# Performance work log

Hardware: AMD Instinct MI355X
Metric: run time of the kernel (lower is better)

Reference implementation:

```python
import jax, jax.numpy as jnp
import numpy as np
from math import factorial

N_NODES = 100000
N_EDGES = 1600000
HIDDEN = 8
N_GRAPHS = 64
RC = 1.5            # PolynomialCutoff radius
CUT_P = 6           # polynomial cutoff exponent (DimeNet-style)
GB_SIGMA = 0.1      # GaussianBasisExpansion width
GB_NUM = 10
GB_LO, GB_HI = 0.7, 1.7
LN2 = 0.6931471805599453

def _cgc(j1, m1, j2, m2, j3, m3):
    if m1 + m2 != m3:
        return 0.0
    f = factorial
    pre = ((2*j3+1) * f(j3+j1-j2) * f(j3-j1+j2) * f(j1+j2-j3) / f(j1+j2+j3+1)) ** 0.5
    pre *= (f(j3+m3)*f(j3-m3)*f(j1-m1)*f(j1+m1)*f(j2-m2)*f(j2+m2)) ** 0.5
    s = 0.0
    for k in range(max(0, j2-j3-m1, j1-j3+m2), min(j1+j2-j3, j1-m1, j2+m2) + 1):
        s += (-1)**k / (f(k)*f(j1+j2-j3-k)*f(j1-m1-k)*f(j2+m2-k)*f(j3-j2+m1+k)*f(j3-j1-m2+k))
    return pre * s

def _u(l):
    # complex -> real spherical-harmonic change of basis; rows indexed by real m = -l..l
    U = np.zeros((2*l+1, 2*l+1), dtype=complex)
    U[l, l] = 1.0
    for m in range(1, l+1):
        U[l+m, l+m] = (-1)**m / np.sqrt(2.0)
        U[l+m, l-m] = 1.0 / np.sqrt(2.0)
        U[l-m, l-m] = 1j / np.sqrt(2.0)
        U[l-m, l+m] = -1j * (-1)**m / np.sqrt(2.0)
    return U

def _real_cg(l1, l2, l3):
    cgc = np.zeros((2*l1+1, 2*l2+1, 2*l3+1), dtype=complex)
    for m1 in range(-l1, l1+1):
        for m2 in range(-l2, l2+1):
            m3 = m1 + m2
            if -l3 <= m3 <= l3:
                cgc[l1+m1, l2+m2, l3+m3] = _cgc(l1, m1, l2, m2, l3, m3)
    W = np.einsum('ai,bj,ck,ijk->cab', _u(l1), _u(l2), np.conj(_u(l3)), cgc)
    re, im = np.real(W), np.imag(W)
    w = re if np.abs(re).sum() >= np.abs(im).sum() else im
    return jnp.asarray(w, dtype=jnp.float32)  # (2l3+1, 2l1+1, 2l2+1)

_TRIPLES = [(0,0,0),(0,1,1),(1,0,1),(1,1,0),(1,1,1),(1,2,1)]
CG = {t: _real_cg(*t) for t in _TRIPLES}
PATHS1 = [(0,0,0),(0,1,1)]                                    # L_in=0, L_edge=2, L_out=1
PATHS2 = [(0,0,0),(0,1,1),(1,0,1),(1,1,0),(1,1,1),(1,2,1)]    # L_in=1, L_edge=2, L_out=1
PATHS3 = [(0,0,0),(1,1,0)]                                    # L_in=1, L_edge=2, L_out=0
DEG_L1 = jnp.array([0, 1, 1, 1])  # degree of each order slot for L = 0..1
DEG_L0 = jnp.array([0])

def _ssp(x):
    return jax.nn.softplus(x) - LN2

def _so3_linear(x, sh, w, paths, n_out_orders, channel_wise):
    # x: (E, in_orders, Cin); sh: (E, edge_orders); w: (E,P,C) or (E,P,Cin,Cout)
    E = x.shape[0]
    c_out = w.shape[-1]
    out = jnp.zeros((E, n_out_orders, c_out), x.dtype)
    for p, (l1, l2, l3) in enumerate(paths):
        cg = CG[(l1, l2, l3)]                      # (2l3+1, 2l1+1, 2l2+1)
        xs = x[:, l1*l1:(l1+1)**2, :]
        ss = sh[:, l2*l2:(l2+1)**2]
        m = jnp.einsum('oab,eac,eb->eoc', cg, xs, ss)
        if channel_wise:
            m = m * w[:, p][:, None, :]
        else:
            m = jnp.einsum('eoc,ecd->eod', m, w[:, p])
        out = out.at[:, l3*l3:(l3+1)**2, :].add(m)
    return out

def _norm_act(h, act, degs):
    # NormAct: per-degree, per-channel norm gating x * act(||x||) / ||x||
    parts = []
    for l in degs:
        seg = h[:, l*l:(l+1)**2, :]
        n = jnp.sqrt(jnp.sum(seg*seg, axis=1, keepdims=True) + 1e-12)
        parts.append(seg * (act(n) / n))
    return jnp.concatenate(parts, axis=1)

def _tfn_block(x, src, dst, sh, edge_emb, edge_w, wp_w, wp_b, si_w, paths, n_out_orders, channel_wise, deg_idx):
    E = sh.shape[0]
    c_in = x.shape[-1]
    lw = edge_emb @ wp_w + wp_b                  # weight_producer (per-edge CG path weights)
    P = len(paths)
    if channel_wise:
        lw = lw.reshape(E, P, c_in)
    else:
        lw = lw.reshape(E, P, c_in, -1)
    msg = _so3_linear(x[src], sh, lw, paths, n_out_orders, channel_wise)  # gather + CG TP
    msg = msg * edge_w[:, None, None]
    agg = jax.ops.segment_sum(msg, dst, num_segments=N_NODES)             # scatter-sum
    return jnp.einsum('nmc,mcd->nmd', agg, si_w[deg_idx])                 # DegreeWiseLinear self-interaction

def _forward(x, edge_index, edge_sh, edge_len, batch, wp1_w, wp1_b, wp2_w, wp2_b, wp3_w, wp3_b, si1_w, si2_w, si3_w, out_w, out_b):
    src, dst = edge_index[0], edge_index[1]
    centers = jnp.linspace(GB_LO, GB_HI, GB_NUM)
    edge_emb = jnp.exp(-(edge_len[:, None] - centers[None, :])**2 / (2.0 * GB_SIGMA**2))
    u = edge_len / RC
    p = CUT_P
    cut = 1.0 - (p+1)*(p+2)/2.0*u**p + p*(p+2)*u**(p+1) - p*(p+1)/2.0*u**(p+2)
    edge_w = jnp.where(u < 1.0, cut, 0.0)
    h = x[:, None, :]                                   # (N, 1 order, 1 channel)
    h = _tfn_block(h, src, dst, edge_sh, edge_emb, edge_w, wp1_w, wp1_b, si1_w, PATHS1, 4, False, DEG_L1)
    h = _norm_act(h, _ssp, (0, 1))
    h = _tfn_block(h, src, dst, edge_sh, edge_emb, edge_w, wp2_w, wp2_b, si2_w, PATHS2, 4, True, DEG_L1)
    h = _norm_act(h, _ssp, (0, 1))
    h = _tfn_block(h, src, dst, edge_sh, edge_emb, edge_w, wp3_w, wp3_b, si3_w, PATHS3, 1, True, DEG_L0)
    h = jax.nn.silu(h)
    g = jax.ops.segment_sum(h[:, 0, :], batch, num_segments=N_GRAPHS)   # SumAggregation pool
    return jax.nn.softmax(g @ out_w + out_b, axis=-1)

def setup_inputs():
    key = jax.random.key(0)
    ks = jax.random.split(key, 16)
    H = HIDDEN
    s = lambda k, shp: jax.random.normal(k, shp, jnp.float32) * 0.1
    return {
        'x': jax.random.normal(ks[0], (N_NODES, 1), jnp.float32),
        'edge_index': jax.random.randint(ks[1], (2, N_EDGES), 0, N_NODES),
        'edge_sh': jax.random.normal(ks[2], (N_EDGES, 9), jnp.float32),
        'edge_len': jax.random.uniform(ks[3], (N_EDGES,), jnp.float32) * 1.5,
        'batch': jnp.sort(jax.random.randint(ks[4], (N_NODES,), 0, N_GRAPHS)),
        'wp1_w': s(ks[5], (10, 2*H)), 'wp1_b': jnp.zeros((2*H,), jnp.float32),
        'wp2_w': s(ks[6], (10, 6*H)), 'wp2_b': jnp.zeros((6*H,), jnp.float32),
        'wp3_w': s(ks[7], (10, 2*H)), 'wp3_b': jnp.zeros((2*H,), jnp.float32),
        'si1_w': s(ks[8], (2, H, H)), 'si2_w': s(ks[9], (2, H, H)), 'si3_w': s(ks[10], (1, H, H)),
        'out_w': s(ks[11], (H, 8)), 'out_b': jnp.zeros((8,), jnp.float32),
    }

def reference(x, edge_index, edge_sh, edge_len, batch, wp1_w, wp1_b, wp2_w, wp2_b, wp3_w, wp3_b, si1_w, si2_w, si3_w, out_w, out_b):
    return _forward(x, edge_index, edge_sh, edge_len, batch, wp1_w, wp1_b, wp2_w, wp2_b, wp3_w, wp3_b, si1_w, si2_w, si3_w, out_w, out_b)
```

## Files before the change

kernel.cpp:

```cpp
#include <hip/hip_runtime.h>
#include <hip/hip_fp16.h>
#include <math.h>
#include <complex>

#define NN 100000
#define NE 1600000
#define NG 64
#define TBINS 256
#define NBLK_E   6250
#define NBLK_N8  3125
#define NBLK_SCAN 391

struct CGTables {
  float c000;
  float c011[3][3];
  float c101[3][3];
  float c110[3][3];
  float c111[3][3][3];
  float c121[3][3][5];
};
struct CGConsts {
  float c000;
  float l011, l101, l110, l111;
  float s121[5][5];
};

static double hfact(int n){ double r=1.0; for(int i=2;i<=n;++i) r*=(double)i; return r; }

static double host_cgc(int j1,int m1,int j2,int m2,int j3,int m3){
  if (m1+m2 != m3) return 0.0;
  double pre = sqrt((2.0*j3+1.0)*hfact(j3+j1-j2)*hfact(j3-j1+j2)*hfact(j1+j2-j3)/hfact(j1+j2+j3+1));
  pre *= sqrt(hfact(j3+m3)*hfact(j3-m3)*hfact(j1-m1)*hfact(j1+m1)*hfact(j2-m2)*hfact(j2+m2));
  int k0 = 0; if (j2-j3-m1 > k0) k0 = j2-j3-m1; if (j1-j3+m2 > k0) k0 = j1-j3+m2;
  int k1 = j1+j2-j3; if (j1-m1 < k1) k1 = j1-m1; if (j2+m2 < k1) k1 = j2+m2;
  double s = 0.0;
  for (int k=k0;k<=k1;++k){
    double t = 1.0/(hfact(k)*hfact(j1+j2-j3-k)*hfact(j1-m1-k)*hfact(j2+m2-k)*hfact(j3-j2+m1+k)*hfact(j3-j1-m2+k));
    s += (k&1) ? -t : t;
  }
  return pre*s;
}

typedef std::complex<double> cd;

static void host_u(int l, cd U[5][5]){
  for (int a=0;a<5;++a) for (int b=0;b<5;++b) U[a][b] = 0.0;
  U[l][l] = 1.0;
  const double is2 = 1.0/sqrt(2.0);
  for (int m=1;m<=l;++m){
    double sgn = (m&1) ? -1.0 : 1.0;
    U[l+m][l+m] = sgn*is2;
    U[l+m][l-m] = is2;
    U[l-m][l-m] = cd(0.0, is2);
    U[l-m][l+m] = cd(0.0, -sgn*is2);
  }
}

static void host_real_cg(int l1,int l2,int l3, float* out){
  cd U1[5][5], U2[5][5], U3[5][5];
  host_u(l1,U1); host_u(l2,U2); host_u(l3,U3);
  int n1=2*l1+1, n2=2*l2+1, n3=2*l3+1;
  double cgt[5][5][5];
  for (int i=0;i<5;++i) for (int j=0;j<5;++j) for (int k=0;k<5;++k) cgt[i][j][k]=0.0;
  for (int m1=-l1;m1<=l1;++m1) for (int m2=-l2;m2<=l2;++m2){
    int m3 = m1+m2;
    if (m3 >= -l3 && m3 <= l3) cgt[l1+m1][l2+m2][l3+m3] = host_cgc(l1,m1,l2,m2,l3,m3);
  }
  cd W[5][5][5];
  double sre=0.0, sim=0.0;
  for (int c=0;c<n3;++c) for (int a=0;a<n1;++a) for (int b=0;b<n2;++b){
    cd acc = 0.0;
    for (int i=0;i<n1;++i) for (int j=0;j<n2;++j) for (int k=0;k<n3;++k)
      acc += U1[a][i]*U2[b][j]*std::conj(U3[c][k])*cgt[i][j][k];
    W[c][a][b] = acc;
    sre += fabs(acc.real()); sim += fabs(acc.imag());
  }
  bool use_re = (sre >= sim);
  for (int c=0;c<n3;++c) for (int a=0;a<n1;++a) for (int b=0;b<n2;++b)
    out[(c*n1+a)*n2+b] = (float)(use_re ? W[c][a][b].real() : W[c][a][b].imag());
}

static void build_cg_tables(CGTables& t){
  float w000[1];  host_real_cg(0,0,0,w000); t.c000 = w000[0];
  float w011[9];  host_real_cg(0,1,1,w011);
  for (int o=0;o<3;++o) for (int b=0;b<3;++b) t.c011[o][b] = w011[o*3+b];
  float w101[9];  host_real_cg(1,0,1,w101);
  for (int o=0;o<3;++o) for (int a=0;a<3;++a) t.c101[o][a] = w101[o*3+a];
  float w110[9];  host_real_cg(1,1,0,w110);
  for (int a=0;a<3;++a) for (int b=0;b<3;++b) t.c110[a][b] = w110[a*3+b];
  float w111[27]; host_real_cg(1,1,1,w111);
  for (int o=0;o<3;++o) for (int a=0;a<3;++a) for (int b=0;b<3;++b) t.c111[o][a][b] = w111[(o*3+a)*3+b];
  float w121[45]; host_real_cg(1,2,1,w121);
  for (int o=0;o<3;++o) for (int a=0;a<3;++a) for (int b=0;b<5;++b) t.c121[o][a][b] = w121[(o*3+a)*5+b];
}

static void build_cg_consts(const CGTables& t, CGConsts& K){
  K.c000 = t.c000;
  K.l011 = t.c011[0][0];
  K.l101 = t.c101[0][0];
  K.l110 = t.c110[0][0];
  K.l111 = t.c111[0][1][2];
  const int pi[5] = {0,0,0,1,1};
  const int pj[5] = {0,1,2,1,2};
  for (int p=0;p<5;++p)
    for (int b=0;b<5;++b)
      K.s121[p][b] = 0.5f*(t.c121[pi[p]][pj[p]][b] + t.c121[pj[p]][pi[p]][b]);
}

__device__ __forceinline__ float sspf(float v){
  float sp = (v > 30.0f) ? v : log1pf(expf(v));
  return sp - 0.69314718055994531f;
}

__device__ __forceinline__ float cutoff_w(float len){
  float u = len * (1.0f/1.5f);
  float u2 = u*u, u6 = u2*u2*u2, u7 = u6*u, u8 = u7*u;
  float cut = 1.0f - 28.0f*u6 + 48.0f*u7 - 21.0f*u8;
  return (u < 1.0f) ? cut : 0.0f;
}

__device__ __forceinline__ float pack2h(float a, float b){
  __half2 h = __floats2half2_rn(a, b);
  return *reinterpret_cast<float*>(&h);
}
__device__ __forceinline__ float2 unpack2h(float f){
  __half2 h = *reinterpret_cast<__half2*>(&f);
  return __half22float2(h);
}

__global__ __launch_bounds__(256) void lwtab_kernel(
    const float* __restrict__ wpw, const float* __restrict__ wpb,
    int NP, float* __restrict__ tab)
{
  int idx = blockIdx.x*256 + threadIdx.x;
  int tot = TBINS*NP*8;
  if (idx >= tot) return;
  int stride = NP*8;
  int bin = idx / stride;
  int r = idx - bin*stride;
  float len = (1.5f/(TBINS-1)) * bin;
  float v = wpb[r];
  #pragma unroll
  for (int i=0;i<10;++i){
    float dd = len - (0.7f + (float)i*(1.0f/9.0f));
    v = fmaf(wpw[i*stride + r], __expf(-50.0f*dd*dd), v);
  }
  tab[idx] = v;
}

__global__ __launch_bounds__(256) void hist_kernel(const int* __restrict__ dst, int* __restrict__ hist){
  int e = blockIdx.x*256 + threadIdx.x;
  if (e >= NE) return;
  atomicAdd(&hist[dst[e]], 1);
}

__global__ __launch_bounds__(256) void scan1_kernel(const int* __restrict__ hist, int* __restrict__ bsum){
  __shared__ int s[256];
  int i = blockIdx.x*256 + threadIdx.x;
  int t = threadIdx.x;
  s[t] = (i < NN) ? hist[i] : 0;
  __syncthreads();
  for (int off=128; off>0; off>>=1){ if (t < off) s[t] += s[t+off]; __syncthreads(); }
  if (t == 0) bsum[blockIdx.x] = s[0];
}

__global__ __launch_bounds__(512) void scan2_kernel(const int* __restrict__ bsum, int* __restrict__ boff){
  __shared__ int s[512];
  int t = threadIdx.x;
  int v = (t < NBLK_SCAN) ? bsum[t] : 0;
  s[t] = v; __syncthreads();
  for (int off=1; off<512; off<<=1){
    int u = (t >= off) ? s[t-off] : 0;
    __syncthreads();
    s[t] += u;
    __syncthreads();
  }
  if (t < NBLK_SCAN) boff[t] = s[t] - v;
}

__global__ __launch_bounds__(256) void scan3_kernel(const int* __restrict__ hist, const int* __restrict__ boff,
                                                   int* __restrict__ rowptr, int* __restrict__ cursor){
  __shared__ int s[256];
  int i = blockIdx.x*256 + threadIdx.x;
  int t = threadIdx.x;
  int v = (i < NN) ? hist[i] : 0;
  s[t] = v; __syncthreads();
  for (int off=1; off<256; off<<=1){
    int u = (t >= off) ? s[t-off] : 0;
    __syncthreads();
    s[t] += u;
    __syncthreads();
  }
  int excl = s[t] - v + boff[blockIdx.x];
  if (i < NN){ rowptr[i] = excl; cursor[i] = excl; }
  if (i == 0) rowptr[NN] = NE;
}

__global__ __launch_bounds__(256) void deg_hist_kernel(const int* __restrict__ rowptr, int* __restrict__ dcnt){
  __shared__ int lb[256];
  lb[threadIdx.x] = 0; __syncthreads();
  int n = blockIdx.x*256 + threadIdx.x;
  if (n < NN){
    int d = rowptr[n+1]-rowptr[n]; if (d > 255) d = 255;
    atomicAdd(&lb[d], 1);
  }
  __syncthreads();
  if (lb[threadIdx.x]) atomicAdd(&dcnt[threadIdx.x], lb[threadIdx.x]);
}

__global__ void deg_scan_kernel(const int* __restrict__ dcnt, int* __restrict__ dcur){
  __shared__ int s[256];
  int t = threadIdx.x;
  int v = dcnt[t];
  s[t] = v; __syncthreads();
  for (int off=1; off<256; off<<=1){
    int u = (t >= off) ? s[t-off] : 0;
    __syncthreads();
    s[t] += u;
    __syncthreads();
  }
  dcur[t] = s[t] - v;
}

__global__ __launch_bounds__(256) void deg_scatter_kernel(const int* __restrict__ rowptr,
                                                          int* __restrict__ dcur, int* __restrict__ perm){
  __shared__ int lcnt[256];
  __shared__ int lbase[256];
  int t = threadIdx.x;
  lcnt[t] = 0;
  __syncthreads();
  int n = blockIdx.x*256 + t;
  int d = 0, lrank = 0;
  bool valid = (n < NN);
  if (valid){
    d = rowptr[n+1]-rowptr[n]; if (d > 255) d = 255;
    lrank = atomicAdd(&lcnt[d], 1);
  }
  __syncthreads();
  int cnt = lcnt[t];
  if (cnt > 0) lbase[t] = atomicAdd(&dcur[t], cnt);
  __syncthreads();
  if (valid) perm[lbase[d] + lrank] = n;
}

__global__ __launch_bounds__(256) void scatter_rec_kernel(
    const int* __restrict__ src, const int* __restrict__ dst,
    const float* __restrict__ sh, const float* __restrict__ elen,
    const float* __restrict__ x,
    int* __restrict__ cursor, float4* __restrict__ rec, CGConsts K)
{
  int e = blockIdx.x*256 + threadIdx.x;
  if (e >= NE) return;
  float len = elen[e];
  float w = cutoff_w(len);
  const float* shr = sh + (size_t)e*9;
  float sh0 = shr[0]*w, shx = shr[1]*w, shy = shr[2]*w, shz = shr[3]*w;
  float b0 = shr[4], b1 = shr[5], b2 = shr[6], b3 = shr[7], b4 = shr[8];
  float S[5];
  #pragma unroll
  for (int p=0;p<5;++p)
    S[p] = (K.s121[p][0]*b0 + K.s121[p][1]*b1 + K.s121[p][2]*b2 + K.s121[p][3]*b3 + K.s121[p][4]*b4)*w;
  int sn = src[e];
  float x0 = x[sn];
  int d = dst[e];
  int slot = atomicAdd(&cursor[d], 1);
  float4* rp = rec + (size_t)slot*2;
  rp[0] = make_float4(__int_as_float(sn), len, pack2h(sh0, shx), pack2h(shy, shz));
  rp[1] = make_float4(pack2h(S[0], S[1]), pack2h(S[2], S[3]), S[4], x0);
}

__global__ __launch_bounds__(256) void gather1_kernel(
    const int* __restrict__ rowptr, const int* __restrict__ perm,
    const float4* __restrict__ rec, const float* __restrict__ tab,
    const float* __restrict__ si, float* __restrict__ out, CGConsts K)
{
  __shared__ float lwt[TBINS*16];
  for (int i=threadIdx.x; i<TBINS*16; i+=256) lwt[i] = tab[i];
  __syncthreads();
  int gid = blockIdx.x*256 + threadIdx.x;
  int c = gid & 7;
  int n = perm[gid >> 3];
  int r0 = rowptr[n], r1 = rowptr[n+1];
  float a0=0.f, a1=0.f, a2=0.f, a3=0.f;
  #pragma unroll 2
  for (int s=r0; s<r1; ++s){
    const float4* rp = rec + (size_t)s*2;
    float4 q0 = rp[0];
    float4 q1 = rp[1];
    float len = q0.y;
    float2 s01 = unpack2h(q0.z);
    float2 s23 = unpack2h(q0.w);
    float sh0 = s01.x, shx = s01.y, shy = s23.x, shz = s23.y;
    float x0 = q1.w;
    float fb = len * ((TBINS-1)/1.5f);
    int bin = (int)fb; if (bin > TBINS-2) bin = TBINS-2;
    float fr = fb - (float)bin;
    int tb = bin*16 + c;
    float lw0 = fmaf(fr, lwt[tb+16]-lwt[tb], lwt[tb]);
    float lw1 = fmaf(fr, lwt[tb+24]-lwt[tb+8], lwt[tb+8]);
    a0 = fmaf(K.c000*sh0, x0*lw0, a0);
    float t = K.l011*x0*lw1;
    a1 = fmaf(t, shx, a1); a2 = fmaf(t, shy, a2); a3 = fmaf(t, shz, a3);
  }
  float z0=0.f, z1=0.f, z2=0.f, z3=0.f;
  #pragma unroll
  for (int k=0;k<8;++k){
    float y0 = __shfl(a0,k,8), y1 = __shfl(a1,k,8), y2 = __shfl(a2,k,8), y3 = __shfl(a3,k,8);
    float w0 = si[k*8+c], w1 = si[64+k*8+c];
    z0 = fmaf(y0,w0,z0); z1 = fmaf(y1,w1,z1); z2 = fmaf(y2,w1,z2); z3 = fmaf(y3,w1,z3);
  }
  float n0 = sqrtf(z0*z0 + 1e-12f);
  float r0v = z0*(sspf(n0)/n0);
  float nv = sqrtf(z1*z1 + z2*z2 + z3*z3 + 1e-12f);
  float sc = sspf(nv)/nv;
  float4 o = make_float4(r0v, z1*sc, z2*sc, z3*sc);
  *reinterpret_cast<float4*>(out + ((size_t)n*8 + c)*4) = o;
}

__global__ __launch_bounds__(256) void gather2_kernel(
    const float* __restrict__ hin,
    const int* __restrict__ rowptr, const int* __restrict__ perm,
    const float4* __restrict__ rec, const float* __restrict__ tab,
    const float* __restrict__ si, float* __restrict__ out, CGConsts K)
{
  __shared__ float lwt[TBINS*48];
  for (int i=threadIdx.x; i<TBINS*48; i+=256) lwt[i] = tab[i];
  __syncthreads();
  int gid = blockIdx.x*256 + threadIdx.x;
  int c = gid & 7;
  int n = perm[gid >> 3];
  int r0 = rowptr[n], r1 = rowptr[n+1];
  float a0=0.f, a1=0.f, a2=0.f, a3=0.f;
  #pragma unroll 2
  for (int s=r0; s<r1; ++s){
    const float4* rp = rec + (size_t)s*2;
    float4 q0 = rp[0];
    float4 q1 = rp[1];
    int sn = __float_as_int(q0.x);
    float len = q0.y;
    float2 s01 = unpack2h(q0.z);
    float2 s23 = unpack2h(q0.w);
    float sh0 = s01.x, shx = s01.y, shy = s23.x, shz = s23.y;
    float2 Sa = unpack2h(q1.x);
    float2 Sb = unpack2h(q1.y);
    float S00 = Sa.x, S01 = Sa.y, S02 = Sb.x, S11 = Sb.y, S12 = q1.z;
    float S22 = -S00 - S11;
    float4 hv = *reinterpret_cast<const float4*>(hin + ((size_t)sn*8 + c)*4);
    float x0 = hv.x, xa0 = hv.y, xa1 = hv.z, xa2 = hv.w;
    float fb = len * ((TBINS-1)/1.5f);
    int bin = (int)fb; if (bin > TBINS-2) bin = TBINS-2;
    float fr = fb - (float)bin;
    int tb = bin*48 + c;
    float lw[6];
    #pragma unroll
    for (int p=0;p<6;++p){
      float t0v = lwt[tb + p*8];
      float t1v = lwt[tb + 48 + p*8];
      lw[p] = fmaf(fr, t1v - t0v, t0v);
    }
    float shdotx = shx*xa0 + shy*xa1 + shz*xa2;
    a0 += K.c000*sh0*x0*lw[0] + K.l110*shdotx*lw[3];
    float t011 = K.l011*x0*lw[1];
    float t101 = K.l101*sh0*lw[2];
    float l4 = K.l111*lw[4];
    float sx0 = S00*xa0 + S01*xa1 + S02*xa2;
    float sx1 = S01*xa0 + S11*xa1 + S12*xa2;
    float sx2 = S02*xa0 + S12*xa1 + S22*xa2;
    a1 += t011*shx + t101*xa0 + l4*(xa1*shz - xa2*shy) + sx0*lw[5];
    a2 += t011*shy + t101*xa1 + l4*(xa2*shx - xa0*shz) + sx1*lw[5];
    a3 += t011*shz + t101*xa2 + l4*(xa0*shy - xa1*shx) + sx2*lw[5];
  }
  float z0=0.f, z1=0.f, z2=0.f, z3=0.f;
  #pragma unroll
  for (int k=0;k<8;++k){
    float y0 = __shfl(a0,k,8), y1 = __shfl(a1,k,8), y2 = __shfl(a2,k,8), y3 = __shfl(a3,k,8);
    float w0 = si[k*8+c], w1 = si[64+k*8+c];
    z0 = fmaf(y0,w0,z0); z1 = fmaf(y1,w1,z1); z2 = fmaf(y2,w1,z2); z3 = fmaf(y3,w1,z3);
  }
  float n0 = sqrtf(z0*z0 + 1e-12f);
  float r0v = z0*(sspf(n0)/n0);
  float nv = sqrtf(z1*z1 + z2*z2 + z3*z3 + 1e-12f);
  float sc = sspf(nv)/nv;
  float4 o = make_float4(r0v, z1*sc, z2*sc, z3*sc);
  *reinterpret_cast<float4*>(out + ((size_t)n*8 + c)*4) = o;
}

__global__ __launch_bounds__(256) void gather3_kernel(
    const float* __restrict__ hin, const int* __restrict__ rowptr, const int* __restrict__ perm,
    const float4* __restrict__ rec, const float* __restrict__ tab,
    const float* __restrict__ si, const int* __restrict__ batch,
    float* __restrict__ G, CGConsts K)
{
  __shared__ float lwt[TBINS*16];
  __shared__ float lg[512];
  for (int i=threadIdx.x; i<TBINS*16; i+=256) lwt[i] = tab[i];
  lg[threadIdx.x] = 0.f; lg[256+threadIdx.x] = 0.f;
  __syncthreads();
  int gid = blockIdx.x*256 + threadIdx.x;
  int c = gid & 7;
  int n = perm[gid >> 3];
  int r0 = rowptr[n], r1 = rowptr[n+1];
  float acc = 0.f;
  #pragma unroll 2
  for (int s=r0; s<r1; ++s){
    float4 q0 = rec[(size_t)s*2];
    int sn = __float_as_int(q0.x);
    float len = q0.y;
    float2 s01 = unpack2h(q0.z);
    float2 s23 = unpack2h(q0.w);
    float sh0 = s01.x, shx = s01.y, shy = s23.x, shz = s23.y;
    float4 hv = *reinterpret_cast<const float4*>(hin + ((size_t)sn*8 + c)*4);
    float fb = len * ((TBINS-1)/1.5f);
    int bin = (int)fb; if (bin > TBINS-2) bin = TBINS-2;
    float fr = fb - (float)bin;
    int tb = bin*16 + c;
    float lw0 = fmaf(fr, lwt[tb+16]-lwt[tb], lwt[tb]);
    float lw1 = fmaf(fr, lwt[tb+24]-lwt[tb+8], lwt[tb+8]);
    float shdotx = shx*hv.y + shy*hv.z + shz*hv.w;
    acc += K.c000*sh0*hv.x*lw0 + K.l110*shdotx*lw1;
  }
  float z = 0.f;
  #pragma unroll
  for (int k=0;k<8;++k){
    float y = __shfl(acc,k,8);
    z = fmaf(y, si[k*8+c], z);
  }
  float v = z / (1.0f + expf(-z));
  atomicAdd(&lg[batch[n]*8 + c], v);
  __syncthreads();
  int t = threadIdx.x;
  float v0 = lg[t];     if (v0 != 0.f) unsafeAtomicAdd(&G[t], v0);
  float v1 = lg[256+t]; if (v1 != 0.f) unsafeAtomicAdd(&G[256+t], v1);
}

__global__ void final_kernel(
    const float* __restrict__ g, const float* __restrict__ ow,
    const float* __restrict__ ob, float* __restrict__ out)
{
  int i = threadIdx.x;
  if (i >= NG) return;
  float gv[8];
  #pragma unroll
  for (int c=0;c<8;++c) gv[c] = g[i*8+c];
  float lg[8];
  #pragma unroll
  for (int j=0;j<8;++j){
    float acc = ob[j];
    #pragma unroll
    for (int c=0;c<8;++c) acc += gv[c]*ow[c*8+j];
    lg[j] = acc;
  }
  float mx = lg[0];
  #pragma unroll
  for (int j=1;j<8;++j) mx = fmaxf(mx, lg[j]);
  float ssum = 0.0f;
  #pragma unroll
  for (int j=0;j<8;++j){ lg[j] = expf(lg[j]-mx); ssum += lg[j]; }
  float inv = 1.0f/ssum;
  #pragma unroll
  for (int j=0;j<8;++j) out[i*8+j] = lg[j]*inv;
}

__global__ __launch_bounds__(256) void edge1_kernel(
    const float* __restrict__ x, const int* __restrict__ src, const int* __restrict__ dst,
    const float* __restrict__ sh, const float* __restrict__ elen,
    const float* __restrict__ wpw, const float* __restrict__ wpb,
    float* __restrict__ agg, CGTables cg)
{
  __shared__ float sw[176];
  for (int i=threadIdx.x;i<176;i+=256) sw[i] = (i<160) ? wpw[i] : wpb[i-160];
  __syncthreads();
  int e = blockIdx.x*256 + threadIdx.x;
  if (e >= NE) return;
  float len = elen[e];
  float lw[16];
  #pragma unroll
  for (int j=0;j<16;++j) lw[j] = sw[160+j];
  #pragma unroll
  for (int i=0;i<10;++i){
    float dd = len - (0.7f + (float)i*(1.0f/9.0f));
    float em = __expf(-50.0f*dd*dd);
    #pragma unroll
    for (int j=0;j<16;++j) lw[j] += em*sw[i*16+j];
  }
  float w = cutoff_w(len);
  int s = src[e], d = dst[e];
  float x0 = x[s];
  const float* shr = sh + (size_t)e*9;
  float sh0 = shr[0], sh1 = shr[1], sh2 = shr[2], sh3 = shr[3];
  float* ag = agg + (size_t)d*32;
  float b0 = cg.c000*x0*sh0*w;
  #pragma unroll
  for (int j=0;j<8;++j) unsafeAtomicAdd(ag+j, b0*lw[j]);
  #pragma unroll
  for (int o=0;o<3;++o){
    float s011 = cg.c011[o][0]*sh1 + cg.c011[o][1]*sh2 + cg.c011[o][2]*sh3;
    float bo = s011*x0*w;
    #pragma unroll
    for (int j=0;j<8;++j) unsafeAtomicAdd(ag+(1+o)*8+j, bo*lw[8+j]);
  }
}

__global__ __launch_bounds__(256) void edge2_kernel(
    const float* __restrict__ h, const int* __restrict__ src, const int* __restrict__ dst,
    const float* __restrict__ sh, const float* __restrict__ elen,
    const float* __restrict__ wpw, const float* __restrict__ wpb,
    float* __restrict__ agg, CGTables cg)
{
  __shared__ float sw[528];
  for (int i=threadIdx.x;i<528;i+=256) sw[i] = (i<480) ? wpw[i] : wpb[i-480];
  __syncthreads();
  int e = blockIdx.x*256 + threadIdx.x;
  if (e >= NE) return;
  float len = elen[e];
  float lw[48];
  #pragma unroll
  for (int j=0;j<48;++j) lw[j] = sw[480+j];
  #pragma unroll
  for (int i=0;i<10;++i){
    float dd = len - (0.7f + (float)i*(1.0f/9.0f));
    float em = __expf(-50.0f*dd*dd);
    #pragma unroll
    for (int j=0;j<48;++j) lw[j] += em*sw[i*48+j];
  }
  float w = cutoff_w(len);
  int s = src[e], d = dst[e];
  float shv[9];
  const float* shr = sh + (size_t)e*9;
  #pragma unroll
  for (int i=0;i<9;++i) shv[i] = shr[i];
  float sh0 = shv[0];
  float s011[3], k110[3], k111[3][3], k121[3][3];
  #pragma unroll
  for (int o=0;o<3;++o) s011[o] = cg.c011[o][0]*shv[1] + cg.c011[o][1]*shv[2] + cg.c011[o][2]*shv[3];
  #pragma unroll
  for (int a=0;a<3;++a) k110[a] = cg.c110[a][0]*shv[1] + cg.c110[a][1]*shv[2] + cg.c110[a][2]*shv[3];
  #pragma unroll
  for (int o=0;o<3;++o)
    #pragma unroll
    for (int a=0;a<3;++a)
      k111[o][a] = cg.c111[o][a][0]*shv[1] + cg.c111[o][a][1]*shv[2] + cg.c111[o][a][2]*shv[3];
  #pragma unroll
  for (int o=0;o<3;++o)
    #pragma unroll
    for (int a=0;a<3;++a){
      float acc = 0.0f;
      #pragma unroll
      for (int b=0;b<5;++b) acc += cg.c121[o][a][b]*shv[4+b];
      k121[o][a] = acc;
    }
  const float4* hr = reinterpret_cast<const float4*>(h + (size_t)s*32);
  float xs[32];
  #pragma unroll
  for (int i=0;i<8;++i){
    float4 q = hr[i];
    xs[i*4] = q.x; xs[i*4+1] = q.y; xs[i*4+2] = q.z; xs[i*4+3] = q.w;
  }
  float* ag = agg + (size_t)d*32;
  #pragma unroll
  for (int c=0;c<8;++c){
    float x0 = xs[c], x1 = xs[8+c], x2 = xs[16+c], x3 = xs[24+c];
    float r0 = cg.c000*sh0*x0*lw[c]
             + (k110[0]*x1 + k110[1]*x2 + k110[2]*x3)*lw[24+c];
    unsafeAtomicAdd(ag+c, r0*w);
    #pragma unroll
    for (int o=0;o<3;++o){
      float r = s011[o]*x0*lw[8+c]
              + (cg.c101[o][0]*x1 + cg.c101[o][1]*x2 + cg.c101[o][2]*x3)*sh0*lw[16+c]
              + (k111[o][0]*x1 + k111[o][1]*x2 + k111[o][2]*x3)*lw[32+c]
              + (k121[o][0]*x1 + k121[o][1]*x2 + k121[o][2]*x3)*lw[40+c];
      unsafeAtomicAdd(ag+(1+o)*8+c, r*w);
    }
  }
}

__global__ __launch_bounds__(256) void edge3_kernel(
    const float* __restrict__ h, const int* __restrict__ src, const int* __restrict__ dst,
    const float* __restrict__ sh, const float* __restrict__ elen,
    const float* __restrict__ wpw, const float* __restrict__ wpb,
    float* __restrict__ agg, CGTables cg)
{
  __shared__ float sw[176];
  for (int i=threadIdx.x;i<176;i+=256) sw[i] = (i<160) ? wpw[i] : wpb[i-160];
  __syncthreads();
  int e = blockIdx.x*256 + threadIdx.x;
  if (e >= NE) return;
  float len = elen[e];
  float lw[16];
  #pragma unroll
  for (int j=0;j<16;++j) lw[j] = sw[160+j];
  #pragma unroll
  for (int i=0;i<10;++i){
    float dd = len - (0.7f + (float)i*(1.0f/9.0f));
    float em = __expf(-50.0f*dd*dd);
    #pragma unroll
    for (int j=0;j<16;++j) lw[j] += em*sw[i*16+j];
  }
  float w = cutoff_w(len);
  int s = src[e], d = dst[e];
  const float* shr = sh + (size_t)e*9;
  float sh0 = shr[0], sh1 = shr[1], sh2 = shr[2], sh3 = shr[3];
  float k110[3];
  #pragma unroll
  for (int a=0;a<3;++a) k110[a] = cg.c110[a][0]*sh1 + cg.c110[a][1]*sh2 + cg.c110[a][2]*sh3;
  const float4* hr = reinterpret_cast<const float4*>(h + (size_t)s*32);
  float xs[32];
  #pragma unroll
  for (int i=0;i<8;++i){
    float4 q = hr[i];
    xs[i*4] = q.x; xs[i*4+1] = q.y; xs[i*4+2] = q.z; xs[i*4+3] = q.w;
  }
  float* ag = agg + (size_t)d*8;
  #pragma unroll
  for (int c=0;c<8;++c){
    float r = cg.c000*sh0*xs[c]*lw[c]
            + (k110[0]*xs[8+c] + k110[1]*xs[16+c] + k110[2]*xs[24+c])*lw[8+c];
    unsafeAtomicAdd(ag+c, r*w);
  }
}

__global__ __launch_bounds__(256) void node_fb_kernel(
    const float* __restrict__ agg, const float* __restrict__ si,
    float* __restrict__ out)
{
  __shared__ float s_si[128];
  if (threadIdx.x < 128) s_si[threadIdx.x] = si[threadIdx.x];
  __syncthreads();
  int idx = blockIdx.x*256 + threadIdx.x;
  if (idx >= NN*8) return;
  int n = idx >> 3, d = idx & 7;
  const float* ar = agg + (size_t)n*32;
  float y[4];
  #pragma unroll
  for (int m=0;m<4;++m){
    const float* sm = s_si + (m ? 64 : 0);
    float acc = 0.0f;
    #pragma unroll
    for (int c=0;c<8;++c) acc += ar[m*8+c]*sm[c*8+d];
    y[m] = acc;
  }
  float n0 = sqrtf(y[0]*y[0] + 1e-12f);
  float r0 = y[0]*(sspf(n0)/n0);
  float n1 = sqrtf(y[1]*y[1] + y[2]*y[2] + y[3]*y[3] + 1e-12f);
  float sc = sspf(n1)/n1;
  float* orow = out + (size_t)n*32;
  orow[d]      = r0;
  orow[8+d]    = y[1]*sc;
  orow[16+d]   = y[2]*sc;
  orow[24+d]   = y[3]*sc;
}

__global__ __launch_bounds__(256) void node3_fb_kernel(
    const float* __restrict__ agg, const float* __restrict__ si,
    const int* __restrict__ batch, float* __restrict__ g)
{
  __shared__ float s_si[64];
  if (threadIdx.x < 64) s_si[threadIdx.x] = si[threadIdx.x];
  __syncthreads();
  int n = blockIdx.x*256 + threadIdx.x;
  if (n >= NN) return;
  const float* ar = agg + (size_t)n*8;
  float av[8];
  #pragma unroll
  for (int c=0;c<8;++c) av[c] = ar[c];
  int b = batch[n];
  float* gr = g + (size_t)b*8;
  #pragma unroll
  for (int d=0;d<8;++d){
    float acc = 0.0f;
    #pragma unroll
    for (int c=0;c<8;++c) acc += av[c]*s_si[c*8+d];
    float v = acc / (1.0f + expf(-acc));
    unsafeAtomicAdd(gr+d, v);
  }
}

extern "C" void kernel_launch(void* const* d_in, const int* in_sizes, int n_in,
                              void* d_out, int out_size, void* d_ws, size_t ws_size,
                              hipStream_t stream)
{
  const float* x     = (const float*)d_in[0];
  const int*   eidx  = (const int*)  d_in[1];
  const float* esh   = (const float*)d_in[2];
  const float* elen  = (const float*)d_in[3];
  const int*   batch = (const int*)  d_in[4];
  const float* wp1w  = (const float*)d_in[5];
  const float* wp1b  = (const float*)d_in[6];
  const float* wp2w  = (const float*)d_in[7];
  const float* wp2b  = (const float*)d_in[8];
  const float* wp3w  = (const float*)d_in[9];
  const float* wp3b  = (const float*)d_in[10];
  const float* si1   = (const float*)d_in[11];
  const float* si2   = (const float*)d_in[12];
  const float* si3   = (const float*)d_in[13];
  const float* outw  = (const float*)d_in[14];
  const float* outb  = (const float*)d_in[15];
  const int* src = eidx;
  const int* dst = eidx + NE;

  CGTables cg;
  build_cg_tables(cg);
  CGConsts K;
  build_cg_consts(cg, K);

  char* p = (char*)d_ws;
  auto carve = [&](size_t bytes) -> void* {
    void* r = (void*)p;
    p += ((bytes + 255)/256)*256;
    return r;
  };
  int*    rowptr = (int*)   carve((NN+1)*4);
  int*    cursor = (int*)   carve(NN*4);
  int*    hist   = (int*)   carve(NN*4);
  int*    perm   = (int*)   carve(NN*4);
  int*    bsum   = (int*)   carve(512*4);
  int*    boff   = (int*)   carve(512*4);
  int*    dcnt   = (int*)   carve(256*4);
  int*    dcur   = (int*)   carve(256*4);
  float*  tab1   = (float*) carve(TBINS*16*4);
  float*  tab2   = (float*) carve(TBINS*48*4);
  float*  tab3   = (float*) carve(TBINS*16*4);
  float4* rec    = (float4*)carve((size_t)NE*32);
  float*  B1     = (float*) carve((size_t)NN*32*4);
  float*  B2     = (float*) carve((size_t)NN*32*4);
  float*  G      = (float*) carve(512*4);
  size_t need = (size_t)(p - (char*)d_ws);

  if (ws_size >= need){
    hipMemsetAsync(hist, 0, NN*sizeof(int), stream);
    hipMemsetAsync(dcnt, 0, 256*sizeof(int), stream);
    hipMemsetAsync(G, 0, 512*sizeof(float), stream);
    lwtab_kernel<<<(TBINS*16+255)/256, 256, 0, stream>>>(wp1w, wp1b, 2, tab1);
    lwtab_kernel<<<(TBINS*48+255)/256, 256, 0, stream>>>(wp2w, wp2b, 6, tab2);
    lwtab_kernel<<<(TBINS*16+255)/256, 256, 0, stream>>>(wp3w, wp3b, 2, tab3);
    hist_kernel<<<NBLK_E, 256, 0, stream>>>(dst, hist);
    scan1_kernel<<<NBLK_SCAN, 256, 0, stream>>>(hist, bsum);
    scan2_kernel<<<1, 512, 0, stream>>>(bsum, boff);
    scan3_kernel<<<NBLK_SCAN, 256, 0, stream>>>(hist, boff, rowptr, cursor);
    deg_hist_kernel<<<NBLK_SCAN, 256, 0, stream>>>(rowptr, dcnt);
    deg_scan_kernel<<<1, 256, 0, stream>>>(dcnt, dcur);
    deg_scatter_kernel<<<NBLK_SCAN, 256, 0, stream>>>(rowptr, dcur, perm);
    scatter_rec_kernel<<<NBLK_E, 256, 0, stream>>>(src, dst, esh, elen, x, cursor, rec, K);
    gather1_kernel<<<NBLK_N8, 256, 0, stream>>>(rowptr, perm, rec, tab1, si1, B1, K);
    gather2_kernel<<<NBLK_N8, 256, 0, stream>>>(B1, rowptr, perm, rec, tab2, si2, B2, K);
    gather3_kernel<<<NBLK_N8, 256, 0, stream>>>(B2, rowptr, perm, rec, tab3, si3, batch, G, K);
    final_kernel<<<1, 64, 0, stream>>>(G, outw, outb, (float*)d_out);
  } else {
    float* A  = (float*)d_ws;
    float* Bf = A + (size_t)NN*32;
    float* Cf = Bf + (size_t)NN*32;
    float* Gf = Cf + (size_t)NN*8;
    hipMemsetAsync(A, 0, (size_t)NN*32*sizeof(float), stream);
    edge1_kernel<<<NBLK_E, 256, 0, stream>>>(x, src, dst, esh, elen, wp1w, wp1b, A, cg);
    node_fb_kernel<<<(NN*8+255)/256, 256, 0, stream>>>(A, si1, Bf);
    hipMemsetAsync(A, 0, (size_t)NN*32*sizeof(float), stream);
    edge2_kernel<<<NBLK_E, 256, 0, stream>>>(Bf, src, dst, esh, elen, wp2w, wp2b, A, cg);
    node_fb_kernel<<<(NN*8+255)/256, 256, 0, stream>>>(A, si2, Bf);
    hipMemsetAsync(Cf, 0, (size_t)NN*8*sizeof(float), stream);
    edge3_kernel<<<NBLK_E, 256, 0, stream>>>(Bf, src, dst, esh, elen, wp3w, wp3b, Cf, cg);
    hipMemsetAsync(Gf, 0, (size_t)NG*8*sizeof(float), stream);
    node3_fb_kernel<<<(NN+255)/256, 256, 0, stream>>>(Cf, si3, batch, Gf);
    final_kernel<<<1, 64, 0, stream>>>(Gf, outw, outb, (float*)d_out);
  }
}
```

Measured before the change: 314.9 us.

## Replace per-node atomic CSR build with two-level bucket sort of edge records

Builds the destination-sorted edge records in two passes: a coarse bucket histogram/scan over 128-node buckets, a block-local scatter into bucket ranges, then a per-bucket in-shared-memory counting sort that writes the final sorted records and rowptr. The aim is to remove the global per-node atomic histogram, the three-kernel scan, and the fully random per-edge scatter writes, replacing them with more coherent writes at the cost of an extra full copy of the edge records. The local destination index is packed into the upper bits of the source index, so gathers now mask it out. It also halves the layer-2 radial lookup table resolution, which shrinks shared memory but changes interpolation accuracy slightly.

```diff
diff --git a/kernel.cpp b/kernel.cpp
--- a/kernel.cpp
+++ b/kernel.cpp
@@ -6,7 +6,12 @@
 #define NN 100000
 #define NE 1600000
 #define NG 64
+#define NBUCK 782
+#define SCB 256
+#define SEB 6250
 #define TBINS 256
+#define TB2   128
+#define MAXB  2560
 #define NBLK_E   6250
 #define NBLK_N8  3125
 #define NBLK_SCAN 391
@@ -130,15 +135,15 @@
 
 __global__ __launch_bounds__(256) void lwtab_kernel(
     const float* __restrict__ wpw, const float* __restrict__ wpb,
-    int NP, float* __restrict__ tab)
+    int NP, int bins, float* __restrict__ tab)
 {
   int idx = blockIdx.x*256 + threadIdx.x;
-  int tot = TBINS*NP*8;
+  int tot = bins*NP*8;
   if (idx >= tot) return;
   int stride = NP*8;
   int bin = idx / stride;
   int r = idx - bin*stride;
-  float len = (1.5f/(TBINS-1)) * bin;
+  float len = (1.5f/(bins-1)) * bin;
   float v = wpb[r];
   #pragma unroll
   for (int i=0;i<10;++i){
@@ -148,52 +153,129 @@
   tab[idx] = v;
 }
 
-__global__ __launch_bounds__(256) void hist_kernel(const int* __restrict__ dst, int* __restrict__ hist){
-  int e = blockIdx.x*256 + threadIdx.x;
-  if (e >= NE) return;
-  atomicAdd(&hist[dst[e]], 1);
-}
-
-__global__ __launch_bounds__(256) void scan1_kernel(const int* __restrict__ hist, int* __restrict__ bsum){
-  __shared__ int s[256];
-  int i = blockIdx.x*256 + threadIdx.x;
+__global__ __launch_bounds__(256) void bhist_kernel(const int* __restrict__ dst, int* __restrict__ bcnt){
+  __shared__ int cnt[NBUCK];
+  for (int j=threadIdx.x; j<NBUCK; j+=256) cnt[j] = 0;
+  __syncthreads();
+  int base = blockIdx.x * SEB;
+  for (int i=threadIdx.x; i<SEB; i+=256)
+    atomicAdd(&cnt[dst[base+i] >> 7], 1);
+  __syncthreads();
+  for (int j=threadIdx.x; j<NBUCK; j+=256)
+    if (cnt[j]) atomicAdd(&bcnt[j], cnt[j]);
+}
+
+__global__ __launch_bounds__(1024) void bscan_kernel(const int* __restrict__ bcnt,
+                                                     int* __restrict__ bbase, int* __restrict__ bclaim){
+  __shared__ int s[1024];
   int t = threadIdx.x;
-  s[t] = (i < NN) ? hist[i] : 0;
-  __syncthreads();
-  for (int off=128; off>0; off>>=1){ if (t < off) s[t] += s[t+off]; __syncthreads(); }
-  if (t == 0) bsum[blockIdx.x] = s[0];
-}
-
-__global__ __launch_bounds__(512) void scan2_kernel(const int* __restrict__ bsum, int* __restrict__ boff){
-  __shared__ int s[512];
-  int t = threadIdx.x;
-  int v = (t < NBLK_SCAN) ? bsum[t] : 0;
+  int v = (t < NBUCK) ? bcnt[t] : 0;
   s[t] = v; __syncthreads();
-  for (int off=1; off<512; off<<=1){
+  for (int off=1; off<1024; off<<=1){
     int u = (t >= off) ? s[t-off] : 0;
     __syncthreads();
     s[t] += u;
     __syncthreads();
   }
-  if (t < NBLK_SCAN) boff[t] = s[t] - v;
-}
-
-__global__ __launch_bounds__(256) void scan3_kernel(const int* __restrict__ hist, const int* __restrict__ boff,
-                                                   int* __restrict__ rowptr, int* __restrict__ cursor){
-  __shared__ int s[256];
-  int i = blockIdx.x*256 + threadIdx.x;
+  if (t < NBUCK){
+    int excl = s[t] - v;
+    bbase[t] = excl;
+    bclaim[t] = excl;
+    if (t == NBUCK-1) bbase[NBUCK] = excl + v;
+  }
+}
+
+__global__ __launch_bounds__(256) void scatter_rec_kernel(
+    const int* __restrict__ src, const int* __restrict__ dst,
+    const float* __restrict__ sh, const float* __restrict__ elen,
+    const float* __restrict__ x,
+    int* __restrict__ bclaim, float4* __restrict__ rec, CGConsts K)
+{
+  __shared__ int cnt[NBUCK];
+  __shared__ int bs[NBUCK];
+  for (int j=threadIdx.x; j<NBUCK; j+=256) cnt[j] = 0;
+  __syncthreads();
+  int base = blockIdx.x * SEB;
+  for (int i=threadIdx.x; i<SEB; i+=256)
+    atomicAdd(&cnt[dst[base+i] >> 7], 1);
+  __syncthreads();
+  for (int j=threadIdx.x; j<NBUCK; j+=256){
+    int c = cnt[j];
+    if (c) bs[j] = atomicAdd(&bclaim[j], c);
+    cnt[j] = 0;
+  }
+  __syncthreads();
+  for (int i=threadIdx.x; i<SEB; i+=256){
+    int e = base + i;
+    int d = dst[e];
+    int b = d >> 7;
+    int off = atomicAdd(&cnt[b], 1);
+    int slot = bs[b] + off;
+    float len = elen[e];
+    float w = cutoff_w(len);
+    const float* shr = sh + (size_t)e*9;
+    float sh0 = shr[0]*w, shx = shr[1]*w, shy = shr[2]*w, shz = shr[3]*w;
+    float b0 = shr[4], b1 = shr[5], b2 = shr[6], b3 = shr[7], b4 = shr[8];
+    float S[5];
+    #pragma unroll
+    for (int p=0;p<5;++p)
+      S[p] = (K.s121[p][0]*b0 + K.s121[p][1]*b1 + K.s121[p][2]*b2 + K.s121[p][3]*b3 + K.s121[p][4]*b4)*w;
+    int sn = src[e];
+    float x0 = x[sn];
+    int packed = sn | ((d & 127) << 20);
+    float4* rp = rec + (size_t)slot*2;
+    rp[0] = make_float4(__int_as_float(packed), len, pack2h(sh0, shx), pack2h(shy, shz));
+    rp[1] = make_float4(pack2h(S[0], S[1]), pack2h(S[2], S[3]), S[4], x0);
+  }
+}
+
+__global__ __launch_bounds__(256) void sortcopy_kernel(
+    const float4* __restrict__ recin, const int* __restrict__ bbase,
+    float4* __restrict__ recout, int* __restrict__ rowptr)
+{
+  __shared__ int hist[128], offs[128], cur[128];
+  __shared__ short outmap[MAXB];
+  int b = blockIdx.x;
+  int e0 = bbase[b], e1 = bbase[b+1];
+  int cnt = e1 - e0;
   int t = threadIdx.x;
-  int v = (i < NN) ? hist[i] : 0;
-  s[t] = v; __syncthreads();
-  for (int off=1; off<256; off<<=1){
-    int u = (t >= off) ? s[t-off] : 0;
+  if (t < 128) hist[t] = 0;
+  __syncthreads();
+  for (int i=t; i<cnt; i+=256){
+    int packed = __float_as_int(recin[(size_t)(e0+i)*2].x);
+    atomicAdd(&hist[packed >> 20], 1);
+  }
+  __syncthreads();
+  if (t < 128) offs[t] = hist[t];
+  __syncthreads();
+  for (int off=1; off<128; off<<=1){
+    int v = (t < 128 && t >= off) ? offs[t-off] : 0;
     __syncthreads();
-    s[t] += u;
+    if (t < 128) offs[t] += v;
     __syncthreads();
   }
-  int excl = s[t] - v + boff[blockIdx.x];
-  if (i < NN){ rowptr[i] = excl; cursor[i] = excl; }
-  if (i == 0) rowptr[NN] = NE;
+  int n0 = b << 7;
+  int nn = NN - n0; if (nn > 128) nn = 128;
+  if (t < 128){
+    int excl = offs[t] - hist[t];
+    cur[t] = excl;
+    if (t < nn) rowptr[n0+t] = e0 + excl;
+  }
+  if (b == NBUCK-1 && t == 0) rowptr[NN] = NE;
+  __syncthreads();
+  for (int i=t; i<cnt; i+=256){
+    int packed = __float_as_int(recin[(size_t)(e0+i)*2].x);
+    int r = atomicAdd(&cur[packed >> 20], 1);
+    outmap[r] = (short)i;
+  }
+  __syncthreads();
+  for (int o=t; o<cnt; o+=256){
+    int j = outmap[o];
+    const float4* rin = recin + (size_t)(e0+j)*2;
+    float4* rout = recout + (size_t)(e0+o)*2;
+    float4 a = rin[0], bq = rin[1];
+    rout[0] = a; rout[1] = bq;
+  }
 }
 
 __global__ __launch_bounds__(256) void deg_hist_kernel(const int* __restrict__ rowptr, int* __restrict__ dcnt){
@@ -241,32 +323,6 @@
   if (cnt > 0) lbase[t] = atomicAdd(&dcur[t], cnt);
   __syncthreads();
   if (valid) perm[lbase[d] + lrank] = n;
-}
-
-__global__ __launch_bounds__(256) void scatter_rec_kernel(
-    const int* __restrict__ src, const int* __restrict__ dst,
-    const float* __restrict__ sh, const float* __restrict__ elen,
-    const float* __restrict__ x,
-    int* __restrict__ cursor, float4* __restrict__ rec, CGConsts K)
-{
-  int e = blockIdx.x*256 + threadIdx.x;
-  if (e >= NE) return;
-  float len = elen[e];
-  float w = cutoff_w(len);
-  const float* shr = sh + (size_t)e*9;
-  float sh0 = shr[0]*w, shx = shr[1]*w, shy = shr[2]*w, shz = shr[3]*w;
-  float b0 = shr[4], b1 = shr[5], b2 = shr[6], b3 = shr[7], b4 = shr[8];
-  float S[5];
-  #pragma unroll
-  for (int p=0;p<5;++p)
-    S[p] = (K.s121[p][0]*b0 + K.s121[p][1]*b1 + K.s121[p][2]*b2 + K.s121[p][3]*b3 + K.s121[p][4]*b4)*w;
-  int sn = src[e];
-  float x0 = x[sn];
-  int d = dst[e];
-  int slot = atomicAdd(&cursor[d], 1);
-  float4* rp = rec + (size_t)slot*2;
-  rp[0] = make_float4(__int_as_float(sn), len, pack2h(sh0, shx), pack2h(shy, shz));
-  rp[1] = make_float4(pack2h(S[0], S[1]), pack2h(S[2], S[3]), S[4], x0);
 }
 
 __global__ __launch_bounds__(256) void gather1_kernel(
@@ -323,8 +379,8 @@
     const float4* __restrict__ rec, const float* __restrict__ tab,
     const float* __restrict__ si, float* __restrict__ out, CGConsts K)
 {
-  __shared__ float lwt[TBINS*48];
-  for (int i=threadIdx.x; i<TBINS*48; i+=256) lwt[i] = tab[i];
+  __shared__ float lwt[TB2*48];
+  for (int i=threadIdx.x; i<TB2*48; i+=256) lwt[i] = tab[i];
   __syncthreads();
   int gid = blockIdx.x*256 + threadIdx.x;
   int c = gid & 7;
@@ -336,7 +392,7 @@
     const float4* rp = rec + (size_t)s*2;
     float4 q0 = rp[0];
     float4 q1 = rp[1];
-    int sn = __float_as_int(q0.x);
+    int sn = __float_as_int(q0.x) & 0xFFFFF;
     float len = q0.y;
     float2 s01 = unpack2h(q0.z);
     float2 s23 = unpack2h(q0.w);
@@ -347,8 +403,8 @@
     float S22 = -S00 - S11;
     float4 hv = *reinterpret_cast<const float4*>(hin + ((size_t)sn*8 + c)*4);
     float x0 = hv.x, xa0 = hv.y, xa1 = hv.z, xa2 = hv.w;
-    float fb = len * ((TBINS-1)/1.5f);
-    int bin = (int)fb; if (bin > TBINS-2) bin = TBINS-2;
+    float fb = len * ((TB2-1)/1.5f);
+    int bin = (int)fb; if (bin > TB2-2) bin = TB2-2;
     float fr = fb - (float)bin;
     int tb = bin*48 + c;
     float lw[6];
@@ -404,7 +460,7 @@
   #pragma unroll 2
   for (int s=r0; s<r1; ++s){
     float4 q0 = rec[(size_t)s*2];
-    int sn = __float_as_int(q0.x);
+    int sn = __float_as_int(q0.x) & 0xFFFFF;
     float len = q0.y;
     float2 s01 = unpack2h(q0.z);
     float2 s23 = unpack2h(q0.w);
@@ -710,40 +766,39 @@
     return r;
   };
   int*    rowptr = (int*)   carve((NN+1)*4);
-  int*    cursor = (int*)   carve(NN*4);
-  int*    hist   = (int*)   carve(NN*4);
   int*    perm   = (int*)   carve(NN*4);
-  int*    bsum   = (int*)   carve(512*4);
-  int*    boff   = (int*)   carve(512*4);
+  int*    bcnt   = (int*)   carve((NBUCK+1)*4);
+  int*    bbase  = (int*)   carve((NBUCK+1)*4);
+  int*    bclaim = (int*)   carve((NBUCK+1)*4);
   int*    dcnt   = (int*)   carve(256*4);
   int*    dcur   = (int*)   carve(256*4);
   float*  tab1   = (float*) carve(TBINS*16*4);
-  float*  tab2   = (float*) carve(TBINS*48*4);
+  float*  tab2   = (float*) carve(TB2*48*4);
   float*  tab3   = (float*) carve(TBINS*16*4);
-  float4* rec    = (float4*)carve((size_t)NE*32);
-  float*  B1     = (float*) carve((size_t)NN*32*4);
-  float*  B2     = (float*) carve((size_t)NN*32*4);
   float*  G      = (float*) carve(512*4);
+  float4* bufX   = (float4*)carve((size_t)NE*32);
+  float4* bufY   = (float4*)carve((size_t)NE*32);
   size_t need = (size_t)(p - (char*)d_ws);
+  float* B1 = (float*)bufX;
+  float* B2 = (float*)bufX + (size_t)NN*32;
 
   if (ws_size >= need){
-    hipMemsetAsync(hist, 0, NN*sizeof(int), stream);
+    hipMemsetAsync(bcnt, 0, (NBUCK+1)*sizeof(int), stream);
     hipMemsetAsync(dcnt, 0, 256*sizeof(int), stream);
     hipMemsetAsync(G, 0, 512*sizeof(float), stream);
-    lwtab_kernel<<<(TBINS*16+255)/256, 256, 0, stream>>>(wp1w, wp1b, 2, tab1);
-    lwtab_kernel<<<(TBINS*48+255)/256, 256, 0, stream>>>(wp2w, wp2b, 6, tab2);
-    lwtab_kernel<<<(TBINS*16+255)/256, 256, 0, stream>>>(wp3w, wp3b, 2, tab3);
-    hist_kernel<<<NBLK_E, 256, 0, stream>>>(dst, hist);
-    scan1_kernel<<<NBLK_SCAN, 256, 0, stream>>>(hist, bsum);
-    scan2_kernel<<<1, 512, 0, stream>>>(bsum, boff);
-    scan3_kernel<<<NBLK_SCAN, 256, 0, stream>>>(hist, boff, rowptr, cursor);
+    lwtab_kernel<<<(TBINS*16+255)/256, 256, 0, stream>>>(wp1w, wp1b, 2, TBINS, tab1);
+    lwtab_kernel<<<(TB2*48+255)/256, 256, 0, stream>>>(wp2w, wp2b, 6, TB2, tab2);
+    lwtab_kernel<<<(TBINS*16+255)/256, 256, 0, stream>>>(wp3w, wp3b, 2, TBINS, tab3);
+    bhist_kernel<<<SCB, 256, 0, stream>>>(dst, bcnt);
+    bscan_kernel<<<1, 1024, 0, stream>>>(bcnt, bbase, bclaim);
+    scatter_rec_kernel<<<SCB, 256, 0, stream>>>(src, dst, esh, elen, x, bclaim, bufX, K);
+    sortcopy_kernel<<<NBUCK, 256, 0, stream>>>(bufX, bbase, bufY, rowptr);
     deg_hist_kernel<<<NBLK_SCAN, 256, 0, stream>>>(rowptr, dcnt);
     deg_scan_kernel<<<1, 256, 0, stream>>>(dcnt, dcur);
     deg_scatter_kernel<<<NBLK_SCAN, 256, 0, stream>>>(rowptr, dcur, perm);
-    scatter_rec_kernel<<<NBLK_E, 256, 0, stream>>>(src, dst, esh, elen, x, cursor, rec, K);
-    gather1_kernel<<<NBLK_N8, 256, 0, stream>>>(rowptr, perm, rec, tab1, si1, B1, K);
-    gather2_kernel<<<NBLK_N8, 256, 0, stream>>>(B1, rowptr, perm, rec, tab2, si2, B2, K);
-    gather3_kernel<<<NBLK_N8, 256, 0, stream>>>(B2, rowptr, perm, rec, tab3, si3, batch, G, K);
+    gather1_kernel<<<NBLK_N8, 256, 0, stream>>>(rowptr, perm, bufY, tab1, si1, B1, K);
+    gather2_kernel<<<NBLK_N8, 256, 0, stream>>>(B1, rowptr, perm, bufY, tab2, si2, B2, K);
+    gather3_kernel<<<NBLK_N8, 256, 0, stream>>>(B2, rowptr, perm, bufY, tab3, si3, batch, G, K);
     final_kernel<<<1, 64, 0, stream>>>(G, outw, outb, (float*)d_out);
   } else {
     float* A  = (float*)d_ws;
```

Result: faster. 263.9 us (-16.2%).
